# Optimization experiments

Measured on AMD Instinct MI355X. Metric: run time of the kernel, lower is better.

The kernel has to match this reference:

```python
import jax, jax.numpy as jnp
import numpy as np

BIG = 10000000.0

def heaviside(x):
    return (jnp.tanh(BIG * x) + 1.0) * 0.5

def interception(Prec, PET, INSC):
    INSC = jnp.clip(INSC * 5.0, 0.5, 5.0)
    IMAX = jnp.maximum(jnp.minimum(INSC, PET), 0.0)
    INT = jnp.maximum(jnp.minimum(IMAX, Prec), 0.0)
    INR = jnp.maximum(Prec - INT, 0.0)
    return INT, INR

def soil_moisture_store(SMS1, SMSC):
    SMSC = jnp.clip(SMSC * 500.0, 50.0, 500.0)
    return jnp.maximum(jnp.minimum(SMS1, SMSC), 0.0)

def soil_fluxes(PET, INT, INR, COEFF, SQ, SMSC, SUB, CRAK, SMS1):
    COEFF = jnp.clip(COEFF * 400.0, 50.0, 400.0)
    SQ = jnp.clip(SQ * 6.0, 0.0, 6.0)
    SMSC = jnp.clip(SMSC * 500.0, 50.0, 500.0)
    SUB = jnp.clip(SUB, 0.0, 1.0)
    CRAK = jnp.clip(CRAK, 0.0, 1.0)
    cap = COEFF * jnp.exp(-SQ * SMS1 / SMSC)
    RMO = jnp.maximum(heaviside(cap - INR) * INR + heaviside(INR - cap) * cap, 0.0)
    IRUN = jnp.maximum(INR - RMO, 0.0)
    SRUN = jnp.maximum(SUB * (SMS1 / SMSC) * RMO, 0.0)
    REC = jnp.maximum(CRAK * (SMS1 / SMSC) * (RMO - SRUN), 0.0)
    SMF = jnp.maximum(RMO - SRUN - REC, 0.0)
    POT = jnp.maximum(PET - INT, 0.0)
    r = 10.0 * SMS1 / SMSC
    ETS = jnp.maximum(heaviside(r - POT) * POT + heaviside(POT - r) * r, 0.0)
    return RMO, IRUN, SRUN, REC, SMF, ETS

def recharge_calculation(SMS1, SMSC, REC, SMF, ETS):
    SMSC = jnp.clip(SMSC * 500.0, 50.0, 500.0)
    s = SMS1 + SMF - ETS
    RECnew = heaviside(s - SMSC) * (REC + s - SMSC) + heaviside(SMSC - s) * REC
    return jnp.maximum(RECnew, 0.0)

def groundwaterstore(GW1, RecK):
    RecK = jnp.clip(RecK * 0.3, 0.003, 0.3)
    return jnp.maximum(heaviside(GW1) * (RecK * GW1), 0.0)

def _forward(inputs, INSC, COEFF, SQ, SMSC, SUB, CRAK, RecK):
    B, T, _ = inputs.shape
    xs = jnp.transpose(inputs, (1, 0, 2))  # (T, B, 2)

    def step(carry, x):
        SMS1, GW1 = carry  # each (B, 1)
        Prec, PET = x[:, 0:1], x[:, 1:2]
        INT, INR = interception(Prec, PET, INSC)
        SMS1c = soil_moisture_store(SMS1, SMSC)
        RMO, IRUN, SRUN, REC, SMF, ETS = soil_fluxes(PET, INT, INR, COEFF, SQ, SMSC, SUB, CRAK, SMS1c)
        next_SMS = SMS1c + jnp.clip(SMF - ETS, -100000.0, 100000.0)
        RECnew = recharge_calculation(SMS1c, SMSC, REC, SMF, ETS)
        BAS = groundwaterstore(GW1, RecK)
        next_GW = GW1 + jnp.clip(RECnew - BAS, -100000.0, 100000.0)
        return (next_SMS, next_GW), jnp.concatenate([next_SMS, next_GW], axis=1)

    init = (jnp.zeros((B, 1), inputs.dtype), jnp.zeros((B, 1), inputs.dtype))
    _, outs = jax.lax.scan(step, init, xs)  # (T, B, 2)
    outs = jnp.transpose(outs, (1, 0, 2))   # (B, T, 2)
    outs = jnp.roll(outs, shift=1, axis=1)  # state at step t-1 (wrap like tf.roll)
    SMS1 = outs[:, :, 0:1]
    GW1 = outs[:, :, 1:2]
    Prec = inputs[:, :, 0:1]
    PET = inputs[:, :, 1:2]
    INT, INR = interception(Prec, PET, INSC)
    SMS1 = soil_moisture_store(SMS1, SMSC)
    RMO, IRUN, SRUN, REC, SMF, ETS = soil_fluxes(PET, INT, INR, COEFF, SQ, SMSC, SUB, CRAK, SMS1)
    RECnew = recharge_calculation(SMS1, SMSC, REC, SMF, ETS)
    BAS = groundwaterstore(GW1, RecK)
    DR = jnp.maximum(SRUN + IRUN, 0.0)
    GD = jnp.maximum(BAS, 0.0)
    Q = jnp.maximum(DR + GD, 0.0)
    return Q  # (B, T, 1)


def setup_inputs() -> dict:
    key = jax.random.key(0)
    k1, = jax.random.split(key, 1)
    B, T = 4096, 1024
    # Prec in [0, 20) mm/day, PET in [0, 8) mm/day
    u = jax.random.uniform(k1, (B, T, 2), dtype=jnp.float32)
    scale = jnp.array([20.0, 8.0], dtype=jnp.float32)
    inputs = u * scale
    p = lambda v: jnp.full((1,), v, dtype=jnp.float32)
    return {
        "inputs": inputs,
        "INSC": p(0.5), "COEFF": p(0.5), "SQ": p(0.5), "SMSC": p(0.5),
        "SUB": p(0.5), "CRAK": p(0.5), "RecK": p(0.5),
    }


def reference(inputs, INSC, COEFF, SQ, SMSC, SUB, CRAK, RecK):
    return _forward(inputs, INSC, COEFF, SQ, SMSC, SUB, CRAK, RecK)
```

## Files before the change

### kernel.cpp

```cpp
#include <hip/hip_runtime.h>
#include <hip/hip_bf16.h>
#include <math.h>


struct P {
    float INSC, SMSC, RecK, g1, lc, k1, k2, k3, c2;
};

__device__ __forceinline__ P make_params(const float* pINSC, const float* pCOEFF,
                                         const float* pSQ,   const float* pSMSC,
                                         const float* pSUB,  const float* pCRAK,
                                         const float* pRecK) {
    P p;
    p.INSC      = fminf(fmaxf(pINSC[0]  * 5.0f,   0.5f),   5.0f);
    float COEFF = fminf(fmaxf(pCOEFF[0] * 400.0f, 50.0f),  400.0f);
    float SQ    = fminf(fmaxf(pSQ[0]    * 6.0f,   0.0f),   6.0f);
    p.SMSC      = fminf(fmaxf(pSMSC[0]  * 500.0f, 50.0f),  500.0f);
    float SUB   = fminf(fmaxf(pSUB[0],  0.0f), 1.0f);
    float CRAK  = fminf(fmaxf(pCRAK[0], 0.0f), 1.0f);
    p.RecK      = fminf(fmaxf(pRecK[0]  * 0.3f,   0.003f), 0.3f);
    p.g1 = 1.0f - p.RecK;
    p.lc = log2f(COEFF);
    float inv = 1.0f / p.SMSC;
    p.k1 = SUB * inv;
    p.k2 = CRAK * inv;
    p.k3 = 10.0f * inv;
    p.c2 = (-SQ * inv) * 1.44269504088896340736f;
    return p;
}

__device__ __forceinline__ float step(float Prec, float PET, float& sms, float& gw, const P& p) {
    float INT  = fminf(fminf(p.INSC, PET), Prec);
    float INR  = Prec - INT;
    float POT  = PET - INT;
    float S    = fminf(sms, p.SMSC);
    float u    = fmaf(-p.k1, S, 1.0f);
    float v    = fmaf(-p.k2, S, 1.0f);
    float ETS  = fminf(POT, p.k3 * S);
    float SmE  = S - ETS;
    float e    = exp2f(fmaf(p.c2, S, p.lc));
    float RMO  = fminf(INR, e);
    float w    = u * RMO;
    float s2   = fmaf(v, w, SmE);
    float SMF  = v * w;
    float REC  = w - SMF;
    float RECnew = REC + fmaxf(s2 - p.SMSC, 0.0f);
    float BAS  = p.RecK * gw;
    float Q    = (INR - w) + BAS;
    gw  = fmaf(p.g1, gw, RECnew);
    sms = s2;
    return Q;
}

__device__ __forceinline__ void stepw(float Prec, float PET, float& sms, float& gw, const P& p) {
    float INT  = fminf(fminf(p.INSC, PET), Prec);
    float INR  = Prec - INT;
    float POT  = PET - INT;
    float S    = fminf(sms, p.SMSC);
    float u    = fmaf(-p.k1, S, 1.0f);
    float v    = fmaf(-p.k2, S, 1.0f);
    float ETS  = fminf(POT, p.k3 * S);
    float SmE  = S - ETS;
    float e    = exp2f(fmaf(p.c2, S, p.lc));
    float RMO  = fminf(INR, e);
    float w    = u * RMO;
    float s2   = fmaf(v, w, SmE);
    float SMF  = v * w;
    float REC  = w - SMF;
    float RECnew = REC + fmaxf(s2 - p.SMSC, 0.0f);
    gw  = fmaf(p.g1, gw, RECnew);
    sms = s2;
}

__device__ __forceinline__ void dstep(float Prec, float PET,
                                      float& slo, float& shi, float& gw, const P& p) {
    float INT = fminf(fminf(p.INSC, PET), Prec);
    float INR = Prec - INT;
    float POT = PET - INT;
    {
        float S    = fminf(shi, p.SMSC);
        float u    = fmaf(-p.k1, S, 1.0f);
        float v    = fmaf(-p.k2, S, 1.0f);
        float ETS  = fminf(POT, p.k3 * S);
        float SmE  = S - ETS;
        float e    = exp2f(fmaf(p.c2, S, p.lc));
        float RMO  = fminf(INR, e);
        float w    = u * RMO;
        float s2   = fmaf(v, w, SmE);
        float SMF  = v * w;
        float REC  = w - SMF;
        float RECnew = REC + fmaxf(s2 - p.SMSC, 0.0f);
        gw  = fmaf(p.g1, gw, RECnew);
        shi = s2;
    }
    {
        float S    = fminf(slo, p.SMSC);
        float u    = fmaf(-p.k1, S, 1.0f);
        float v    = fmaf(-p.k2, S, 1.0f);
        float ETS  = fminf(POT, p.k3 * S);
        float SmE  = S - ETS;
        float e    = exp2f(fmaf(p.c2, S, p.lc));
        float RMO  = fminf(INR, e);
        float w    = u * RMO;
        slo = fmaf(v, w, SmE);
    }
}

#define MERGE_TOL 0.75f


__global__ __launch_bounds__(256)
void transpose_in(const float2* __restrict__ in, float2* __restrict__ tp,
                  int B, int Tdim)
{
    __shared__ float2 tile[64][65];
    int t0 = blockIdx.x * 64, b0 = blockIdx.y * 64;
    int l = threadIdx.x & 63, w = threadIdx.x >> 6;
    #pragma unroll
    for (int j = 0; j < 16; ++j) {
        int bb = w * 16 + j;
        tile[l][bb] = in[(long)(b0 + bb) * Tdim + t0 + l];
    }
    __syncthreads();
    #pragma unroll
    for (int j = 0; j < 16; ++j) {
        int tt = w * 16 + j;
        tp[(long)(t0 + tt) * B + b0 + l] = tile[tt][l];
    }
}

__global__ __launch_bounds__(256)
void transpose_out(const float* __restrict__ qtp, float* __restrict__ out,
                   int B, int Tdim)
{
    __shared__ float tile[64][65];
    int t0 = blockIdx.x * 64, b0 = blockIdx.y * 64;
    int l = threadIdx.x & 63, w = threadIdx.x >> 6;
    #pragma unroll
    for (int j = 0; j < 16; ++j) {
        int tt = w * 16 + j;
        tile[tt][l] = qtp[(long)(t0 + tt) * B + b0 + l];
    }
    __syncthreads();
    #pragma unroll
    for (int j = 0; j < 16; ++j) {
        int bb = w * 16 + j;
        out[(long)(b0 + bb) * Tdim + t0 + l] = tile[l][bb];
    }
}


template<int T, int NC, int W>
__global__ __launch_bounds__(64, 1)
void hir_pass1t(const float2* __restrict__ tp,
                const float* __restrict__ pINSC,  const float* __restrict__ pCOEFF,
                const float* __restrict__ pSQ,    const float* __restrict__ pSMSC,
                const float* __restrict__ pSUB,   const float* __restrict__ pCRAK,
                const float* __restrict__ pRecK,
                float* __restrict__ qtp, float4* __restrict__ st, int B)
{
    int gid = blockIdx.x * blockDim.x + threadIdx.x;
    int b = gid % B;
    int c = gid / B;
    if (c >= NC) return;

    P p = make_params(pINSC, pCOEFF, pSQ, pSMSC, pSUB, pCRAK, pRecK);

    const float2* __restrict__ col = tp + b;

    constexpr int CH = T / NC;
    const int t1 = c * CH;
    int t0 = t1 - W;
    const bool exact = (t0 <= 0);
    if (t0 < 0) t0 = 0;

    float slo = 0.0f, shi = exact ? 0.0f : p.SMSC, gw = 0.0f;

    const int nwb = (t1 - t0) >> 3;
    if (nwb > 0) {
        float2 A[8], Bq[8], C[8];
        #pragma unroll
        for (int j = 0; j < 8; ++j) A[j] = col[(long)(t0 + j) * B];
        {
            int tB = t0 + ((1 < nwb) ? 8 : 0);
            #pragma unroll
            for (int j = 0; j < 8; ++j) Bq[j] = col[(long)(tB + j) * B];
        }
        if (exact) {
            for (int k = 0; k < nwb; ++k) {
                int kn = (k + 2 < nwb) ? (k + 2) : (nwb - 1);
                #pragma unroll
                for (int j = 0; j < 8; ++j) C[j] = col[(long)(t0 + 8 * kn + j) * B];
                #pragma unroll
                for (int j = 0; j < 8; ++j) stepw(A[j].x, A[j].y, shi, gw, p);
                #pragma unroll
                for (int j = 0; j < 8; ++j) { A[j] = Bq[j]; Bq[j] = C[j]; }
            }
            slo = shi;
        } else {
            for (int k = 0; k < nwb; ++k) {
                int kn = (k + 2 < nwb) ? (k + 2) : (nwb - 1);
                #pragma unroll
                for (int j = 0; j < 8; ++j) C[j] = col[(long)(t0 + 8 * kn + j) * B];
                #pragma unroll
                for (int j = 0; j < 8; ++j) dstep(A[j].x, A[j].y, slo, shi, gw, p);
                #pragma unroll
                for (int j = 0; j < 8; ++j) { A[j] = Bq[j]; Bq[j] = C[j]; }
            }
        }
    }
    const bool merged = exact || ((shi - slo) <= MERGE_TOL);
    float sms = exact ? shi : (0.5f * (slo + shi));

    {
        constexpr int nmb = CH / 8;
        float2 A[8], Bq[8], C[8];
        #pragma unroll
        for (int j = 0; j < 8; ++j) A[j] = col[(long)(t1 + j) * B];
        #pragma unroll
        for (int j = 0; j < 8; ++j) Bq[j] = col[(long)(t1 + 8 + j) * B];
        for (int k = 0; k < nmb; ++k) {
            int kn = (k + 2 < nmb) ? (k + 2) : (nmb - 1);
            #pragma unroll
            for (int j = 0; j < 8; ++j) C[j] = col[(long)(t1 + 8 * kn + j) * B];
            int tb = t1 + 8 * k;
            #pragma unroll
            for (int j = 0; j < 8; ++j) {
                float q = step(A[j].x, A[j].y, sms, gw, p);
                int t = tb + j;
                if (!(c == 0 && t == 0)) {
                    qtp[(long)t * B + b] = q;
                }
            }
            #pragma unroll
            for (int j = 0; j < 8; ++j) { A[j] = Bq[j]; Bq[j] = C[j]; }
        }
    }

    st[(size_t)c * B + b] = make_float4(sms, gw, merged ? 1.0f : 0.0f, 0.0f);

    if (c == NC - 1) {
        float2 f0 = col[0];
        float ss = sms, gg = gw;
        qtp[b] = step(f0.x, f0.y, ss, gg, p);
    }
}


__global__ __launch_bounds__(64)
void build_queue(const float4* __restrict__ st, unsigned int* __restrict__ qcount,
                 unsigned int* __restrict__ qitems, int n)
{
    int gid = blockIdx.x * blockDim.x + threadIdx.x;
    bool un = false;
    if (gid < n) un = (st[gid].z == 0.0f);
    unsigned long long mask = __ballot(un);
    int lane = threadIdx.x;
    int cnt = __popcll(mask);
    unsigned int base = 0;
    if (lane == 0 && cnt) base = atomicAdd(qcount, (unsigned int)cnt);
    base = (unsigned int)__shfl((int)base, 0);
    if (un) {
        int pre = __popcll(mask & ((1ull << lane) - 1ull));
        qitems[base + pre] = (unsigned int)gid;
    }
}


template<int T, int NC>
__global__ __launch_bounds__(64)
void hir_fixup(const float* __restrict__ inputs,
               const float* __restrict__ pINSC,  const float* __restrict__ pCOEFF,
               const float* __restrict__ pSQ,    const float* __restrict__ pSMSC,
               const float* __restrict__ pSUB,   const float* __restrict__ pCRAK,
               const float* __restrict__ pRecK,
               float* __restrict__ qtp, const float4* __restrict__ st,
               const unsigned int* __restrict__ qcount,
               const unsigned int* __restrict__ qitems, int B)
{
    int gid = blockIdx.x * blockDim.x + threadIdx.x;
    int stride = gridDim.x * blockDim.x;
    int n = (int)*qcount;

    P p = make_params(pINSC, pCOEFF, pSQ, pSMSC, pSUB, pCRAK, pRecK);
    constexpr int CH = T / NC;

    for (int it = gid; it < n; it += stride) {
        unsigned int item = qitems[it];
        int b = (int)(item % (unsigned int)B);
        int c = (int)(item / (unsigned int)B);

        const float4* __restrict__ rp = (const float4*)(inputs + (size_t)b * (2 * T));

        int m = c - 1;
        float4 sm = st[(size_t)m * B + b];
        while (sm.z == 0.0f) { --m; sm = st[(size_t)m * B + b]; }
        float sms = sm.x, gw = sm.y;

        {
            const int ia = ((m + 1) * CH) >> 1;
            const int ib = (c * CH) >> 1;
            if (ia < ib) {
                float4 cur = rp[ia];
                for (int i = ia; i < ib; ++i) {
                    int ni = (i + 1 < ib) ? (i + 1) : i;
                    float4 nxt = rp[ni];
                    stepw(cur.x, cur.y, sms, gw, p);
                    stepw(cur.z, cur.w, sms, gw, p);
                    cur = nxt;
                }
            }
        }

        {
            const int i1 = (c * CH) >> 1;
            const int i2 = ((c + 1) * CH) >> 1;
            float4 cur = rp[i1];
            for (int i = i1; i < i2; ++i) {
                int ni = (i + 1 < i2) ? (i + 1) : i;
                float4 nxt = rp[ni];
                float qa = step(cur.x, cur.y, sms, gw, p);
                float qb = step(cur.z, cur.w, sms, gw, p);
                qtp[(long)(2 * i) * B + b]     = qa;
                qtp[(long)(2 * i + 1) * B + b] = qb;
                cur = nxt;
            }
        }

        if (c == NC - 1) {
            float4 f0 = rp[0];
            float ss = sms, gg = gw;
            qtp[b] = step(f0.x, f0.y, ss, gg, p);
        }
    }
}


template<int T, int NC, int W>
__global__ __launch_bounds__(64, 1)
void hir_pass1_legacy(const float* __restrict__ inputs,
               const float* __restrict__ pINSC,  const float* __restrict__ pCOEFF,
               const float* __restrict__ pSQ,    const float* __restrict__ pSMSC,
               const float* __restrict__ pSUB,   const float* __restrict__ pCRAK,
               const float* __restrict__ pRecK,
               float* __restrict__ out, float4* __restrict__ st, int B)
{
    int gid = blockIdx.x * blockDim.x + threadIdx.x;
    int b = gid % B;
    int c = gid / B;
    if (c >= NC) return;

    P p = make_params(pINSC, pCOEFF, pSQ, pSMSC, pSUB, pCRAK, pRecK);

    const float4* __restrict__ rp = (const float4*)(inputs + (size_t)b * (2 * T));
    float* __restrict__ orow = out + (size_t)b * T;

    constexpr int CH = T / NC;
    const int i1 = (c * CH) >> 1;
    int i0 = i1 - (W >> 1);
    const bool exact = (i0 <= 0);
    if (i0 < 0) i0 = 0;

    float slo = 0.0f, shi = exact ? 0.0f : p.SMSC, gw = 0.0f;

    const int nwb = (i1 - i0) >> 2;
    if (nwb > 0) {
        float4 A[4], Bq[4], C[4];
        #pragma unroll
        for (int j = 0; j < 4; ++j) A[j] = rp[i0 + j];
        {
            int k1b = (1 < nwb) ? 1 : 0;
            #pragma unroll
            for (int j = 0; j < 4; ++j) Bq[j] = rp[i0 + 4 * k1b + j];
        }
        if (exact) {
            for (int k = 0; k < nwb; ++k) {
                int kn = (k + 2 < nwb) ? (k + 2) : (nwb - 1);
                #pragma unroll
                for (int j = 0; j < 4; ++j) C[j] = rp[i0 + 4 * kn + j];
                #pragma unroll
                for (int j = 0; j < 4; ++j) {
                    stepw(A[j].x, A[j].y, shi, gw, p);
                    stepw(A[j].z, A[j].w, shi, gw, p);
                }
                #pragma unroll
                for (int j = 0; j < 4; ++j) { A[j] = Bq[j]; Bq[j] = C[j]; }
            }
            slo = shi;
        } else {
            for (int k = 0; k < nwb; ++k) {
                int kn = (k + 2 < nwb) ? (k + 2) : (nwb - 1);
                #pragma unroll
                for (int j = 0; j < 4; ++j) C[j] = rp[i0 + 4 * kn + j];
                #pragma unroll
                for (int j = 0; j < 4; ++j) {
                    dstep(A[j].x, A[j].y, slo, shi, gw, p);
                    dstep(A[j].z, A[j].w, slo, shi, gw, p);
                }
                #pragma unroll
                for (int j = 0; j < 4; ++j) { A[j] = Bq[j]; Bq[j] = C[j]; }
            }
        }
    }
    const bool merged = exact || ((shi - slo) <= MERGE_TOL);
    float sms = exact ? shi : (0.5f * (slo + shi));

    {
        constexpr int nmb = (CH / 2) / 4;
        float4 A[4], Bq[4], C[4];
        #pragma unroll
        for (int j = 0; j < 4; ++j) A[j] = rp[i1 + j];
        #pragma unroll
        for (int j = 0; j < 4; ++j) Bq[j] = rp[i1 + 4 + j];
        for (int k = 0; k < nmb; ++k) {
            int kn = (k + 2 < nmb) ? (k + 2) : (nmb - 1);
            #pragma unroll
            for (int j = 0; j < 4; ++j) C[j] = rp[i1 + 4 * kn + j];
            int ibase = i1 + 4 * k;
            #pragma unroll
            for (int j = 0; j < 4; ++j) {
                float qa = step(A[j].x, A[j].y, sms, gw, p);
                float qb = step(A[j].z, A[j].w, sms, gw, p);
                if (c == 0 && k == 0 && j == 0) {
                    orow[1] = qb;
                } else {
                    ((float2*)orow)[ibase + j] = make_float2(qa, qb);
                }
            }
            #pragma unroll
            for (int j = 0; j < 4; ++j) { A[j] = Bq[j]; Bq[j] = C[j]; }
        }
    }

    st[(size_t)c * B + b] = make_float4(sms, gw, merged ? 1.0f : 0.0f, 0.0f);

    if (c == NC - 1) {
        float4 f0 = rp[0];
        float ss = sms, gg = gw;
        orow[0] = step(f0.x, f0.y, ss, gg, p);
    }
}

template<int T, int NC>
__global__ __launch_bounds__(64, 1)
void hir_pass2_legacy(const float* __restrict__ inputs,
               const float* __restrict__ pINSC,  const float* __restrict__ pCOEFF,
               const float* __restrict__ pSQ,    const float* __restrict__ pSMSC,
               const float* __restrict__ pSUB,   const float* __restrict__ pCRAK,
               const float* __restrict__ pRecK,
               float* __restrict__ out, const float4* __restrict__ st, int B)
{
    int b = blockIdx.x * blockDim.x + threadIdx.x;
    if (b >= B) return;

    P p = make_params(pINSC, pCOEFF, pSQ, pSMSC, pSUB, pCRAK, pRecK);
    constexpr int CH = T / NC;

    const float4* __restrict__ rp = (const float4*)(inputs + (size_t)b * (2 * T));
    float* __restrict__ orow = out + (size_t)b * T;

    float4 s0 = st[b];
    float ex_s = s0.x, ex_g = s0.y;

    for (int c = 1; c < NC; ++c) {
        float4 sc = st[(size_t)c * B + b];
        if (sc.z != 0.0f) {
            ex_s = sc.x; ex_g = sc.y;
            continue;
        }
        float sms = ex_s, gw = ex_g;
        const int i1 = (c * CH) >> 1;
        const int i2 = ((c + 1) * CH) >> 1;
        float4 cur = rp[i1];
        for (int i = i1; i < i2; ++i) {
            int ni = (i + 1 < i2) ? (i + 1) : i;
            float4 nxt = rp[ni];
            float qa = step(cur.x, cur.y, sms, gw, p);
            float qb = step(cur.z, cur.w, sms, gw, p);
            ((float2*)orow)[i] = make_float2(qa, qb);
            cur = nxt;
        }
        ex_s = sms; ex_g = gw;
        if (c == NC - 1) {
            float4 f0 = rp[0];
            float ss = sms, gg = gw;
            orow[0] = step(f0.x, f0.y, ss, gg, p);
        }
    }
}

template<int T>
__global__ __launch_bounds__(64, 1)
void hir_scan_kernel(const float* __restrict__ inputs,
                     const float* __restrict__ pINSC,  const float* __restrict__ pCOEFF,
                     const float* __restrict__ pSQ,    const float* __restrict__ pSMSC,
                     const float* __restrict__ pSUB,   const float* __restrict__ pCRAK,
                     const float* __restrict__ pRecK,
                     float* __restrict__ out, int B)
{
    int b = blockIdx.x * blockDim.x + threadIdx.x;
    if (b >= B) return;
    P p = make_params(pINSC, pCOEFF, pSQ, pSMSC, pSUB, pCRAK, pRecK);
    const float4* __restrict__ rp = (const float4*)(inputs + (size_t)b * (2 * T));
    float* __restrict__ orow = out + (size_t)b * T;
    float sms = 0.0f, gw = 0.0f;
    float4 cur = rp[0];
    const float P0 = cur.x, E0 = cur.y;
    constexpr int NI = T / 2;
    for (int i = 0; i < NI; ++i) {
        int ni = (i + 1 < NI) ? (i + 1) : i;
        float4 nxt = rp[ni];
        float qa = step(cur.x, cur.y, sms, gw, p);
        float qb = step(cur.z, cur.w, sms, gw, p);
        if (i == 0) { orow[1] = qb; }
        else        { ((float2*)orow)[i] = make_float2(qa, qb); }
        cur = nxt;
    }
    float ss = sms, gg = gw;
    orow[0] = step(P0, E0, ss, gg, p);
}

extern "C" void kernel_launch(void* const* d_in, const int* in_sizes, int n_in,
                              void* d_out, int out_size, void* d_ws, size_t ws_size,
                              hipStream_t stream) {
    (void)n_in; (void)out_size;
    constexpr int T  = 1024;
    constexpr int NC = 16;
    constexpr int W  = 320;
    const float* inputs = (const float*)d_in[0];
    const float* INSC   = (const float*)d_in[1];
    const float* COEFF  = (const float*)d_in[2];
    const float* SQ     = (const float*)d_in[3];
    const float* SMSC   = (const float*)d_in[4];
    const float* SUB    = (const float*)d_in[5];
    const float* CRAK   = (const float*)d_in[6];
    const float* RecK   = (const float*)d_in[7];
    float* out = (float*)d_out;

    int B = in_sizes[0] / (2 * T);
    size_t tpBytes  = (size_t)B * T * sizeof(float2);
    size_t qtpBytes = (size_t)B * T * sizeof(float);
    size_t stBytes  = (size_t)B * NC * sizeof(float4);
    size_t qBytes   = (size_t)B * NC * sizeof(unsigned int);
    size_t bigNeed  = tpBytes + qtpBytes + stBytes + 64 + qBytes;

    if ((B % 64) == 0 && ws_size >= bigNeed) {
        float2* tp = (float2*)d_ws;
        float*  qtp = (float*)((char*)d_ws + tpBytes);
        float4* st  = (float4*)((char*)d_ws + tpBytes + qtpBytes);
        unsigned int* qcount = (unsigned int*)((char*)d_ws + tpBytes + qtpBytes + stBytes);
        unsigned int* qitems = (unsigned int*)((char*)d_ws + tpBytes + qtpBytes + stBytes + 64);

        hipMemsetAsync(qcount, 0, sizeof(unsigned int), stream);

        transpose_in<<<dim3(T / 64, B / 64), dim3(256), 0, stream>>>(
            (const float2*)inputs, tp, B, T);

        long total = (long)B * NC;
        int blocks1 = (int)((total + 63) / 64);
        hir_pass1t<T, NC, W><<<dim3(blocks1), dim3(64), 0, stream>>>(
            tp, INSC, COEFF, SQ, SMSC, SUB, CRAK, RecK, qtp, st, B);

        build_queue<<<dim3(blocks1), dim3(64), 0, stream>>>(
            st, qcount, qitems, (int)total);

        hir_fixup<T, NC><<<dim3(1024), dim3(64), 0, stream>>>(
            inputs, INSC, COEFF, SQ, SMSC, SUB, CRAK, RecK, qtp, st, qcount, qitems, B);

        transpose_out<<<dim3(T / 64, B / 64), dim3(256), 0, stream>>>(
            qtp, out, B, T);
        return;
    }

    if ((B % 64) == 0 && ws_size >= stBytes) {
        float4* st = (float4*)d_ws;
        long total = (long)B * NC;
        int blocks1 = (int)((total + 63) / 64);
        hir_pass1_legacy<T, NC, W><<<dim3(blocks1), dim3(64), 0, stream>>>(
            inputs, INSC, COEFF, SQ, SMSC, SUB, CRAK, RecK, out, st, B);
        int blocks2 = (B + 63) / 64;
        hir_pass2_legacy<T, NC><<<dim3(blocks2), dim3(64), 0, stream>>>(
            inputs, INSC, COEFF, SQ, SMSC, SUB, CRAK, RecK, out, st, B);
        return;
    }

    int blocks = (B + 63) / 64;
    hir_scan_kernel<T><<<dim3(blocks), dim3(64), 0, stream>>>(
        inputs, INSC, COEFF, SQ, SMSC, SUB, CRAK, RecK, out, B);
}
```

Measured before the change: 145.9 us.

## Split low/high bound warmup across paired lanes and fold counter reset into transpose

Each chunk is now handled by two adjacent lanes: one runs the warmup recurrence from the low bound and the other from the high bound, and they exchange results with a lane shuffle. Previously one thread ran a dual-state step. This doubles thread-level parallelism to shorten the serial per-thread chain, but both lanes then redundantly compute the main chunk, with only one of them storing. The warmup window grows from 320 to 384, trading more work for fewer unmerged chunks that need fixup. The queue counter reset moves from a memset into the transpose kernel, removing one launch.

```diff
diff --git a/kernel.cpp b/kernel.cpp
--- a/kernel.cpp
+++ b/kernel.cpp
@@ -111,8 +111,9 @@
 
 __global__ __launch_bounds__(256)
 void transpose_in(const float2* __restrict__ in, float2* __restrict__ tp,
-                  int B, int Tdim)
-{
+                  unsigned int* __restrict__ qcount, int B, int Tdim)
+{
+    if (blockIdx.x == 0 && blockIdx.y == 0 && threadIdx.x == 0) *qcount = 0u;
     __shared__ float2 tile[64][65];
     int t0 = blockIdx.x * 64, b0 = blockIdx.y * 64;
     int l = threadIdx.x & 63, w = threadIdx.x >> 6;
@@ -160,8 +161,10 @@
                 float* __restrict__ qtp, float4* __restrict__ st, int B)
 {
     int gid = blockIdx.x * blockDim.x + threadIdx.x;
-    int b = gid % B;
-    int c = gid / B;
+    int h  = gid & 1;
+    int pb = gid >> 1;
+    int b = pb % B;
+    int c = pb / B;
     if (c >= NC) return;
 
     P p = make_params(pINSC, pCOEFF, pSQ, pSMSC, pSUB, pCRAK, pRecK);
@@ -174,7 +177,8 @@
     const bool exact = (t0 <= 0);
     if (t0 < 0) t0 = 0;
 
-    float slo = 0.0f, shi = exact ? 0.0f : p.SMSC, gw = 0.0f;
+    float s  = exact ? 0.0f : (h ? 0.0f : p.SMSC);
+    float gw = 0.0f;
 
     const int nwb = (t1 - t0) >> 3;
     if (nwb > 0) {
@@ -186,31 +190,24 @@
             #pragma unroll
             for (int j = 0; j < 8; ++j) Bq[j] = col[(long)(tB + j) * B];
         }
-        if (exact) {
-            for (int k = 0; k < nwb; ++k) {
-                int kn = (k + 2 < nwb) ? (k + 2) : (nwb - 1);
-                #pragma unroll
-                for (int j = 0; j < 8; ++j) C[j] = col[(long)(t0 + 8 * kn + j) * B];
-                #pragma unroll
-                for (int j = 0; j < 8; ++j) stepw(A[j].x, A[j].y, shi, gw, p);
-                #pragma unroll
-                for (int j = 0; j < 8; ++j) { A[j] = Bq[j]; Bq[j] = C[j]; }
-            }
-            slo = shi;
-        } else {
-            for (int k = 0; k < nwb; ++k) {
-                int kn = (k + 2 < nwb) ? (k + 2) : (nwb - 1);
-                #pragma unroll
-                for (int j = 0; j < 8; ++j) C[j] = col[(long)(t0 + 8 * kn + j) * B];
-                #pragma unroll
-                for (int j = 0; j < 8; ++j) dstep(A[j].x, A[j].y, slo, shi, gw, p);
-                #pragma unroll
-                for (int j = 0; j < 8; ++j) { A[j] = Bq[j]; Bq[j] = C[j]; }
-            }
-        }
-    }
+        for (int k = 0; k < nwb; ++k) {
+            int kn = (k + 2 < nwb) ? (k + 2) : (nwb - 1);
+            #pragma unroll
+            for (int j = 0; j < 8; ++j) C[j] = col[(long)(t0 + 8 * kn + j) * B];
+            #pragma unroll
+            for (int j = 0; j < 8; ++j) stepw(A[j].x, A[j].y, s, gw, p);
+            #pragma unroll
+            for (int j = 0; j < 8; ++j) { A[j] = Bq[j]; Bq[j] = C[j]; }
+        }
+    }
+
+    float so = __shfl_xor(s, 1);
+    float go = __shfl_xor(gw, 1);
+    float shi = h ? so : s;
+    float slo = h ? s : so;
+    gw = h ? go : gw;
     const bool merged = exact || ((shi - slo) <= MERGE_TOL);
-    float sms = exact ? shi : (0.5f * (slo + shi));
+    float sms = 0.5f * (slo + shi);
 
     {
         constexpr int nmb = CH / 8;
@@ -228,7 +225,7 @@
             for (int j = 0; j < 8; ++j) {
                 float q = step(A[j].x, A[j].y, sms, gw, p);
                 int t = tb + j;
-                if (!(c == 0 && t == 0)) {
+                if (!h && !(c == 0 && t == 0)) {
                     qtp[(long)t * B + b] = q;
                 }
             }
@@ -237,12 +234,13 @@
         }
     }
 
-    st[(size_t)c * B + b] = make_float4(sms, gw, merged ? 1.0f : 0.0f, 0.0f);
-
-    if (c == NC - 1) {
-        float2 f0 = col[0];
-        float ss = sms, gg = gw;
-        qtp[b] = step(f0.x, f0.y, ss, gg, p);
+    if (!h) {
+        st[(size_t)c * B + b] = make_float4(sms, gw, merged ? 1.0f : 0.0f, 0.0f);
+        if (c == NC - 1) {
+            float2 f0 = col[0];
+            float ss = sms, gg = gw;
+            qtp[b] = step(f0.x, f0.y, ss, gg, p);
+        }
     }
 }
 
@@ -526,7 +524,7 @@
     (void)n_in; (void)out_size;
     constexpr int T  = 1024;
     constexpr int NC = 16;
-    constexpr int W  = 320;
+    constexpr int W  = 384;
     const float* inputs = (const float*)d_in[0];
     const float* INSC   = (const float*)d_in[1];
     const float* COEFF  = (const float*)d_in[2];
@@ -551,18 +549,17 @@
         unsigned int* qcount = (unsigned int*)((char*)d_ws + tpBytes + qtpBytes + stBytes);
         unsigned int* qitems = (unsigned int*)((char*)d_ws + tpBytes + qtpBytes + stBytes + 64);
 
-        hipMemsetAsync(qcount, 0, sizeof(unsigned int), stream);
-
         transpose_in<<<dim3(T / 64, B / 64), dim3(256), 0, stream>>>(
-            (const float2*)inputs, tp, B, T);
-
-        long total = (long)B * NC;
+            (const float2*)inputs, tp, qcount, B, T);
+
+        long total = 2L * B * NC;
         int blocks1 = (int)((total + 63) / 64);
         hir_pass1t<T, NC, W><<<dim3(blocks1), dim3(64), 0, stream>>>(
             tp, INSC, COEFF, SQ, SMSC, SUB, CRAK, RecK, qtp, st, B);
 
-        build_queue<<<dim3(blocks1), dim3(64), 0, stream>>>(
-            st, qcount, qitems, (int)total);
+        int nst = B * NC;
+        build_queue<<<dim3((nst + 63) / 64), dim3(64), 0, stream>>>(
+            st, qcount, qitems, nst);
 
         hir_fixup<T, NC><<<dim3(1024), dim3(64), 0, stream>>>(
             inputs, INSC, COEFF, SQ, SMSC, SUB, CRAK, RecK, qtp, st, qcount, qitems, B);
```

Measured after the change: 157.1 us. +7.7%, slower.
